# Performance work log

Measured on AMD Instinct MI355X. Metric: run time of the kernel, lower is better.

## Reference

```python
import jax, jax.numpy as jnp
import numpy as np

B, LQ, LK, D = 16, 2048, 2048, 64
TEMPERATURE = 8.0


def setup_inputs() -> dict:
    key = jax.random.key(0)
    kq, kk, kv, kt, km = jax.random.split(key, 5)
    q = jax.random.normal(kq, (B, LQ, D), dtype=jnp.float32)
    k = jax.random.normal(kk, (B, LK, D), dtype=jnp.float32)
    v = jax.random.normal(kv, (B, LK, D), dtype=jnp.float32)
    # time differences are positive
    time_diff = jax.random.uniform(kt, (B, LQ, LK), dtype=jnp.float32)
    mask = jax.random.randint(km, (B, LQ, LK), 0, 2).astype(bool)
    time_plus_weight = jnp.zeros((1,), dtype=jnp.float32)
    time_mul_weight = jnp.ones((1,), dtype=jnp.float32)
    return {"q": q, "k": k, "v": v, "time_diff": time_diff, "mask": mask,
            "time_plus_weight": time_plus_weight, "time_mul_weight": time_mul_weight}


def reference(q, k, v, time_diff, mask, time_plus_weight, time_mul_weight):
    # attn = QK^T / temperature  -> [B, LQ, LK]
    attn = jnp.einsum("bqd,bkd->bqk", q, k) / TEMPERATURE
    # time-decay bias (global mean/max over the whole time_diff tensor)
    td = time_diff / jnp.mean(time_diff)
    td = td + jax.nn.softplus(time_plus_weight) * jnp.max(td)
    time_diff_weight = 1.0 / jnp.log(jnp.exp(jnp.float32(1.0)) + td)
    attn = attn + time_mul_weight * time_diff_weight
    attn = jnp.where(mask, jnp.float32(-1e10), attn)
    attn = jax.nn.softmax(attn, axis=2)
    # dropout is identity in eval / p-effective-0 reference
    output = jnp.einsum("bqk,bkd->bqd", attn, v)
    return (output, attn)
```

## Files before the change

### kernel.cpp

```cpp
#include <hip/hip_runtime.h>
#include <hip/hip_bf16.h>

#define B_N 16
#define LQ_N 2048
#define LK_N 2048
#define D_N 64

typedef __attribute__((ext_vector_type(8))) __bf16 bf16x8;
typedef __attribute__((ext_vector_type(4))) float f32x4;
typedef __attribute__((ext_vector_type(2))) unsigned u32x2;
typedef __attribute__((ext_vector_type(4))) unsigned u32x4;

__device__ __forceinline__ unsigned cvt_pk_bf16(float lo, float hi) {
  unsigned r;
  asm("v_cvt_pk_bf16_f32 %0, %1, %2" : "=v"(r) : "v"(lo), "v"(hi));
  return r;
}

__device__ __forceinline__ void gl_lds16(const float* g, float* l) {
  __builtin_amdgcn_global_load_lds(
      (const __attribute__((address_space(1))) void*)g,
      (__attribute__((address_space(3))) void*)l, 16, 0, 0);
}

#define WAIT_VMC(N)  do { asm volatile("s_waitcnt vmcnt(" #N ")" ::: "memory"); __builtin_amdgcn_sched_barrier(0); } while (0)
#define WAIT_LGKM0() do { asm volatile("s_waitcnt lgkmcnt(0)" ::: "memory");    __builtin_amdgcn_sched_barrier(0); } while (0)
#define SBAR()       __builtin_amdgcn_sched_barrier(0)

__global__ __launch_bounds__(256) void red1_kernel(const float* __restrict__ td,
                                                   float* __restrict__ ws) {
  const int tid = threadIdx.x;
  const int gid = blockIdx.x * 256 + tid;
  float s = 0.f, mx = -1e30f;
  const float4* p = reinterpret_cast<const float4*>(td);
  for (int i = gid; i < 16777216; i += 524288) {
    float4 x = p[i];
    s += (x.x + x.y) + (x.z + x.w);
    mx = fmaxf(mx, fmaxf(fmaxf(x.x, x.y), fmaxf(x.z, x.w)));
  }
#pragma unroll
  for (int m = 1; m < 64; m <<= 1) {
    s += __shfl_xor(s, m, 64);
    mx = fmaxf(mx, __shfl_xor(mx, m, 64));
  }
  __shared__ float ss[4], sm[4];
  if ((tid & 63) == 0) { ss[tid >> 6] = s; sm[tid >> 6] = mx; }
  __syncthreads();
  if (tid == 0) {
    ws[blockIdx.x]        = (ss[0] + ss[1]) + (ss[2] + ss[3]);
    ws[2048 + blockIdx.x] = fmaxf(fmaxf(sm[0], sm[1]), fmaxf(sm[2], sm[3]));
  }
}

__global__ __launch_bounds__(256) void red2_kernel(const float* __restrict__ tpw,
                                                   const unsigned* __restrict__ mku,
                                                   float* __restrict__ ws) {
  const int tid = threadIdx.x;
  double s = 0.0; float mx = -1e30f;
  for (int i = tid; i < 2048; i += 256) { s += (double)ws[i]; mx = fmaxf(mx, ws[2048 + i]); }
#pragma unroll
  for (int m = 1; m < 64; m <<= 1) {
    s += __shfl_xor(s, m, 64);
    mx = fmaxf(mx, __shfl_xor(mx, m, 64));
  }
  unsigned big = 0;
  for (int i = tid; i < 1024; i += 256) big |= (mku[i] > 1u) ? 1u : 0u;
  const int anyw = __any(big != 0);
  __shared__ double sd[4]; __shared__ float sm[4]; __shared__ int sa[4];
  if ((tid & 63) == 0) { sd[tid >> 6] = s; sm[tid >> 6] = mx; sa[tid >> 6] = anyw; }
  __syncthreads();
  if (tid == 0) {
    double tot = (sd[0] + sd[1]) + (sd[2] + sd[3]);
    float m4 = fmaxf(fmaxf(sm[0], sm[1]), fmaxf(sm[2], sm[3]));
    double mean = tot / 67108864.0;
    float inv_mean = (float)(1.0 / mean);
    float sp = log1pf(__expf(tpw[0]));
    ws[4096] = inv_mean;
    ws[4097] = sp * m4 * inv_mean;
    ws[4098] = (sa[0] | sa[1] | sa[2] | sa[3]) ? 1.f : 0.f;
    ws[4099] = 2.718281828459045f + sp * m4 * inv_mean;
  }
}

__global__ __launch_bounds__(512)
void attn_kernel(
    const float* __restrict__ q, const float* __restrict__ kp, const float* __restrict__ vp,
    const float* __restrict__ td, const unsigned char* __restrict__ maskb,
    const float* __restrict__ tmwp, const float* __restrict__ ws,
    float* __restrict__ out, float* __restrict__ attn) {

  __shared__ float regA[8][2][1024];
  __shared__ unsigned short Qsb[16 * 72];
  __shared__ unsigned short Ps[8][16 * 24];
  __shared__ float rsum[8][16];

  const int tid  = threadIdx.x;
  const int w    = tid >> 6;
  const int lane = tid & 63;
  const int lrow = lane & 15;
  const int lgrp = lane >> 4;

  const int b     = blockIdx.x >> 7;
  const int qbase = (blockIdx.x & 127) << 4;

  const float inv_mean = ws[4096];
  const float ec       = ws[4099];
  const float tmw      = tmwp[0];
  const float sc       = tmw * 2.0813689810056077f;
  const int   msh      = (ws[4098] != 0.f) ? 0 : 2;

  if (tid < 256) {
    const float qscale = 0.18033688011112042f;
    const int row = tid >> 4, c4 = (tid & 15) << 2;
    f32x4 x = *reinterpret_cast<const f32x4*>(q + ((size_t)(b * LQ_N + qbase + row) << 6) + c4);
    *reinterpret_cast<u32x2*>(&Qsb[row * 72 + c4]) =
        u32x2{ cvt_pk_bf16(x[0] * qscale, x[1] * qscale),
               cvt_pk_bf16(x[2] * qscale, x[3] * qscale) };
  }
  __syncthreads();

  const unsigned qrow = (unsigned)(b * LQ_N + qbase + lrow);
  const unsigned tdo0 = (qrow << 11) + (unsigned)(w * 16 + lgrp * 4);
  const unsigned kvo0 = ((unsigned)b << 17) + ((unsigned)w << 10);
  const unsigned pA = (lgrp << 6) + ((lrow ^ lgrp)       << 2);
  const unsigned pB = (lgrp << 6) + ((lrow ^ (lgrp + 4)) << 2);

  auto dma16 = [&](const float* src_base, int c, int pb) {
    const unsigned base = kvo0 + (unsigned)c * 8192u;
    gl_lds16(src_base + (base         + pA), &regA[w][pb][0]);
    gl_lds16(src_base + (base +  256u + pB), &regA[w][pb][256]);
    gl_lds16(src_base + (base +  512u + pA), &regA[w][pb][512]);
    gl_lds16(src_base + (base +  768u + pB), &regA[w][pb][768]);
  };

  auto ldtd = [&](int c, f32x4* tdv, unsigned* mk4) {
    const unsigned to = tdo0 + (unsigned)c * 128u;
    *tdv = __builtin_nontemporal_load(reinterpret_cast<const f32x4*>(td + to));
    if (msh == 0) {
      *mk4 = *reinterpret_cast<const unsigned*>(maskb + to);
    } else {
      u32x4 m = __builtin_nontemporal_load(
          reinterpret_cast<const u32x4*>(maskb + ((size_t)to << 2)));
      *mk4 = (m[0] & 1u) | ((m[1] & 1u) << 8) | ((m[2] & 1u) << 16) | ((m[3] & 1u) << 24);
    }
  };

  dma16(kp, 0, 0); SBAR();
  dma16(kp, 1, 1); SBAR();
  f32x4    tdb[2];
  unsigned mkb[2];
  ldtd(0, &tdb[0], &mkb[0]); SBAR();

  float rs = 0.f;
  u32x2 E[16];

#pragma unroll
  for (int c = 0; c < 16; ++c) {
    if (c == 0)       { WAIT_VMC(6); }
    else if (c == 15) { WAIT_VMC(4); }
    else              { WAIT_VMC(8); }

    f32x4 acc = {0.f, 0.f, 0.f, 0.f};
#pragma unroll
    for (int h = 0; h < 2; ++h) {
      const int g0 = (h * 8 + lgrp * 2 + 0) ^ (lrow & 7);
      const int g1 = (h * 8 + lgrp * 2 + 1) ^ (lrow & 7);
      f32x4 ka = *(const f32x4*)&regA[w][c & 1][lrow * 64 + g0 * 4];
      f32x4 kc = *(const f32x4*)&regA[w][c & 1][lrow * 64 + g1 * 4];
      bf16x8 qv = *(const bf16x8*)&Qsb[lrow * 72 + h * 32 + lgrp * 8];
      u32x4 kd = { cvt_pk_bf16(ka[0], ka[1]), cvt_pk_bf16(ka[2], ka[3]),
                   cvt_pk_bf16(kc[0], kc[1]), cvt_pk_bf16(kc[2], kc[3]) };
      acc = __builtin_amdgcn_mfma_f32_16x16x32_bf16(__builtin_bit_cast(bf16x8, kd), qv,
                                                    acc, 0, 0, 0);
    }
    WAIT_LGKM0();
    if (c < 14) { dma16(kp, c + 2, c & 1); SBAR(); }
    if (c < 15) { ldtd(c + 1, &tdb[(c + 1) & 1], &mkb[(c + 1) & 1]); SBAR(); }

    if (c <= 13)      { WAIT_VMC(6); }
    else if (c == 14) { WAIT_VMC(2); }
    else              { WAIT_VMC(0); }

    const f32x4    tv  = tdb[c & 1];
    const unsigned mk4 = mkb[c & 1];
    float e4[4];
#pragma unroll
    for (int i = 0; i < 4; ++i) {
      const float z  = __builtin_fmaf(tv[i], inv_mean, ec);
      const float l2 = __builtin_amdgcn_logf(z);
      const float r  = __builtin_amdgcn_rcpf(l2);
      const float sv = __builtin_fmaf(sc, r, acc[i]);
      const float e  = ((mk4 >> (8 * i)) & 0xffu) ? 0.f : __builtin_amdgcn_exp2f(sv);
      e4[i] = e;
      rs += e;
    }
    E[c] = u32x2{ cvt_pk_bf16(e4[0], e4[1]), cvt_pk_bf16(e4[2], e4[3]) };
  }

  dma16(vp, 0, 0); SBAR();
  dma16(vp, 1, 1); SBAR();

  rs += __shfl_xor(rs, 16, 64);
  rs += __shfl_xor(rs, 32, 64);
  if (lgrp == 0) rsum[w][lrow] = rs;
  __syncthreads();
  float invl;
  {
    float s = 0.f;
#pragma unroll
    for (int w2 = 0; w2 < 8; ++w2) s += rsum[w2][lrow];
    invl = __fdividef(1.f, s);
  }

  f32x4 oacc[4];
#pragma unroll
  for (int n = 0; n < 4; ++n) oacc[n] = {0.f, 0.f, 0.f, 0.f};

  const u32x4 zz = {0u, 0u, 0u, 0u};
#pragma unroll
  for (int c = 0; c < 16; ++c) {
    if (c == 0)       { WAIT_VMC(4); }
    else if (c == 1)  { WAIT_VMC(5); }
    else if (c == 15) { WAIT_VMC(2); }
    else              { WAIT_VMC(6); }

    const unsigned ex = E[c][0], ey = E[c][1];
    f32x4 pv;
    pv[0] = __uint_as_float(ex << 16)         * invl;
    pv[1] = __uint_as_float(ex & 0xffff0000u) * invl;
    pv[2] = __uint_as_float(ey << 16)         * invl;
    pv[3] = __uint_as_float(ey & 0xffff0000u) * invl;

    const unsigned d01 = cvt_pk_bf16(pv[0], pv[1]);
    const unsigned d23 = cvt_pk_bf16(pv[2], pv[3]);
    *reinterpret_cast<u32x2*>(&Ps[w][lrow * 24 + lgrp * 4]) = u32x2{ d01, d23 };

    bf16x8 pa;
    if (lgrp < 2) pa = *(const bf16x8*)&Ps[w][lrow * 24 + lgrp * 8];
    else          pa = __builtin_bit_cast(bf16x8, zz);

#pragma unroll
    for (int n = 0; n < 4; ++n) {
      u32x4 vd;
      if (lgrp < 2) {
        float vv[8];
#pragma unroll
        for (int e = 0; e < 8; ++e) {
          const int r    = lgrp * 8 + e;
          const int dcol = n * 16 + lrow;
          const int slot = (dcol >> 2) ^ (r & 7);
          vv[e] = regA[w][c & 1][r * 64 + slot * 4 + (dcol & 3)];
        }
        vd = u32x4{ cvt_pk_bf16(vv[0], vv[1]), cvt_pk_bf16(vv[2], vv[3]),
                    cvt_pk_bf16(vv[4], vv[5]), cvt_pk_bf16(vv[6], vv[7]) };
      } else {
        vd = zz;
      }
      oacc[n] = __builtin_amdgcn_mfma_f32_16x16x32_bf16(pa, __builtin_bit_cast(bf16x8, vd),
                                                        oacc[n], 0, 0, 0);
    }

    WAIT_LGKM0();
    if (c < 14) { dma16(vp, c + 2, c & 1); SBAR(); }

    __builtin_nontemporal_store(pv, reinterpret_cast<f32x4*>(attn + tdo0 + (unsigned)c * 128u));
  }

#pragma unroll
  for (int n = 0; n < 4; ++n)
#pragma unroll
    for (int i = 0; i < 4; ++i)
      regA[w][0][(lgrp * 4 + i) * 64 + n * 16 + lrow] = oacc[n][i];
  __syncthreads();
  for (int i2 = tid; i2 < 1024; i2 += 512) {
    float s = 0.f;
#pragma unroll
    for (int w2 = 0; w2 < 8; ++w2) s += regA[w2][0][i2];
    out[((size_t)(b * LQ_N + qbase) << 6) + i2] = s;
  }
}

extern "C" void kernel_launch(void* const* d_in, const int* in_sizes, int n_in,
                              void* d_out, int out_size, void* d_ws, size_t ws_size,
                              hipStream_t stream) {
  const float* q   = (const float*)d_in[0];
  const float* k   = (const float*)d_in[1];
  const float* v   = (const float*)d_in[2];
  const float* td  = (const float*)d_in[3];
  const unsigned char* mask = (const unsigned char*)d_in[4];
  const float* tpw = (const float*)d_in[5];
  const float* tmw = (const float*)d_in[6];
  float* out  = (float*)d_out;
  float* attn = out + (size_t)B_N * LQ_N * D_N;
  float* wsf  = (float*)d_ws;

  red1_kernel<<<2048, 256, 0, stream>>>(td, wsf);
  red2_kernel<<<1, 256, 0, stream>>>(tpw, (const unsigned*)mask, wsf);
  attn_kernel<<<2048, 512, 0, stream>>>(q, k, v, td, mask, tmw, wsf, out, attn);
}
```

Measured before the change: 322.2 us.

## Split attention into row-sum pass and recompute-emit pass

The fused attention kernel becomes two kernels. The first computes QK^T plus the time bias and writes only the softmax row sums to the workspace. The second recomputes the scores, normalizes them, writes attn and does the PV product, so the E register buffer, the double-buffered K/V LDS region and the shared Q staging are no longer needed. This cuts register and LDS pressure, which could raise occupancy, but it reads time_diff, mask and K twice and runs QK^T twice, adding a lot of global traffic on an already memory-bound problem.

```diff
diff --git a/kernel.cpp b/kernel.cpp
--- a/kernel.cpp
+++ b/kernel.cpp
@@ -26,6 +26,7 @@
 #define WAIT_VMC(N)  do { asm volatile("s_waitcnt vmcnt(" #N ")" ::: "memory"); __builtin_amdgcn_sched_barrier(0); } while (0)
 #define WAIT_LGKM0() do { asm volatile("s_waitcnt lgkmcnt(0)" ::: "memory");    __builtin_amdgcn_sched_barrier(0); } while (0)
 #define SBAR()       __builtin_amdgcn_sched_barrier(0)
+
 
 __global__ __launch_bounds__(256) void red1_kernel(const float* __restrict__ td,
                                                    float* __restrict__ ws) {
@@ -76,22 +77,18 @@
     float inv_mean = (float)(1.0 / mean);
     float sp = log1pf(__expf(tpw[0]));
     ws[4096] = inv_mean;
-    ws[4097] = sp * m4 * inv_mean;
     ws[4098] = (sa[0] | sa[1] | sa[2] | sa[3]) ? 1.f : 0.f;
     ws[4099] = 2.718281828459045f + sp * m4 * inv_mean;
   }
 }
 
 __global__ __launch_bounds__(512)
-void attn_kernel(
-    const float* __restrict__ q, const float* __restrict__ kp, const float* __restrict__ vp,
+void sum_kernel(
+    const float* __restrict__ q, const float* __restrict__ kp,
     const float* __restrict__ td, const unsigned char* __restrict__ maskb,
-    const float* __restrict__ tmwp, const float* __restrict__ ws,
-    float* __restrict__ out, float* __restrict__ attn) {
-
-  __shared__ float regA[8][2][1024];
-  __shared__ unsigned short Qsb[16 * 72];
-  __shared__ unsigned short Ps[8][16 * 24];
+    const float* __restrict__ tmwp, float* __restrict__ ws) {
+
+  __shared__ float Kb[8][1024];
   __shared__ float rsum[8][16];
 
   const int tid  = threadIdx.x;
@@ -109,30 +106,19 @@
   const float sc       = tmw * 2.0813689810056077f;
   const int   msh      = (ws[4098] != 0.f) ? 0 : 2;
 
-  if (tid < 256) {
-    const float qscale = 0.18033688011112042f;
-    const int row = tid >> 4, c4 = (tid & 15) << 2;
-    f32x4 x = *reinterpret_cast<const f32x4*>(q + ((size_t)(b * LQ_N + qbase + row) << 6) + c4);
-    *reinterpret_cast<u32x2*>(&Qsb[row * 72 + c4]) =
-        u32x2{ cvt_pk_bf16(x[0] * qscale, x[1] * qscale),
-               cvt_pk_bf16(x[2] * qscale, x[3] * qscale) };
-  }
-  __syncthreads();
-
   const unsigned qrow = (unsigned)(b * LQ_N + qbase + lrow);
   const unsigned tdo0 = (qrow << 11) + (unsigned)(w * 16 + lgrp * 4);
   const unsigned kvo0 = ((unsigned)b << 17) + ((unsigned)w << 10);
   const unsigned pA = (lgrp << 6) + ((lrow ^ lgrp)       << 2);
   const unsigned pB = (lgrp << 6) + ((lrow ^ (lgrp + 4)) << 2);
 
-  auto dma16 = [&](const float* src_base, int c, int pb) {
+  auto kdma = [&](int c) {
     const unsigned base = kvo0 + (unsigned)c * 8192u;
-    gl_lds16(src_base + (base         + pA), &regA[w][pb][0]);
-    gl_lds16(src_base + (base +  256u + pB), &regA[w][pb][256]);
-    gl_lds16(src_base + (base +  512u + pA), &regA[w][pb][512]);
-    gl_lds16(src_base + (base +  768u + pB), &regA[w][pb][768]);
+    gl_lds16(kp + (base         + pA), &Kb[w][0]);
+    gl_lds16(kp + (base +  256u + pB), &Kb[w][256]);
+    gl_lds16(kp + (base +  512u + pA), &Kb[w][512]);
+    gl_lds16(kp + (base +  768u + pB), &Kb[w][768]);
   };
-
   auto ldtd = [&](int c, f32x4* tdv, unsigned* mk4) {
     const unsigned to = tdo0 + (unsigned)c * 128u;
     *tdv = __builtin_nontemporal_load(reinterpret_cast<const f32x4*>(td + to));
@@ -145,45 +131,55 @@
     }
   };
 
-  dma16(kp, 0, 0); SBAR();
-  dma16(kp, 1, 1); SBAR();
+  const float* qb = q + ((size_t)qrow << 6);
+  f32x4 q0a = *reinterpret_cast<const f32x4*>(qb + lgrp * 8);
+  f32x4 q0b = *reinterpret_cast<const f32x4*>(qb + lgrp * 8 + 4);
+  f32x4 q1a = *reinterpret_cast<const f32x4*>(qb + 32 + lgrp * 8);
+  f32x4 q1b = *reinterpret_cast<const f32x4*>(qb + 32 + lgrp * 8 + 4);
+  SBAR();
+  kdma(0); SBAR();
   f32x4    tdb[2];
   unsigned mkb[2];
   ldtd(0, &tdb[0], &mkb[0]); SBAR();
+  ldtd(1, &tdb[1], &mkb[1]); SBAR();
+
+  WAIT_VMC(8);
+  const float qscale = 0.18033688011112042f;
+  bf16x8 qa[2];
+  {
+    u32x4 k0 = { cvt_pk_bf16(q0a[0]*qscale, q0a[1]*qscale), cvt_pk_bf16(q0a[2]*qscale, q0a[3]*qscale),
+                 cvt_pk_bf16(q0b[0]*qscale, q0b[1]*qscale), cvt_pk_bf16(q0b[2]*qscale, q0b[3]*qscale) };
+    u32x4 k1 = { cvt_pk_bf16(q1a[0]*qscale, q1a[1]*qscale), cvt_pk_bf16(q1a[2]*qscale, q1a[3]*qscale),
+                 cvt_pk_bf16(q1b[0]*qscale, q1b[1]*qscale), cvt_pk_bf16(q1b[2]*qscale, q1b[3]*qscale) };
+    qa[0] = __builtin_bit_cast(bf16x8, k0);
+    qa[1] = __builtin_bit_cast(bf16x8, k1);
+  }
 
   float rs = 0.f;
-  u32x2 E[16];
-
 #pragma unroll
   for (int c = 0; c < 16; ++c) {
-    if (c == 0)       { WAIT_VMC(6); }
-    else if (c == 15) { WAIT_VMC(4); }
-    else              { WAIT_VMC(8); }
+    if (c == 0)       { WAIT_VMC(4); }
+    else if (c == 15) { WAIT_VMC(0); }
+    else              { WAIT_VMC(2); }
 
     f32x4 acc = {0.f, 0.f, 0.f, 0.f};
 #pragma unroll
     for (int h = 0; h < 2; ++h) {
       const int g0 = (h * 8 + lgrp * 2 + 0) ^ (lrow & 7);
       const int g1 = (h * 8 + lgrp * 2 + 1) ^ (lrow & 7);
-      f32x4 ka = *(const f32x4*)&regA[w][c & 1][lrow * 64 + g0 * 4];
-      f32x4 kc = *(const f32x4*)&regA[w][c & 1][lrow * 64 + g1 * 4];
-      bf16x8 qv = *(const bf16x8*)&Qsb[lrow * 72 + h * 32 + lgrp * 8];
+      f32x4 ka = *(const f32x4*)&Kb[w][lrow * 64 + g0 * 4];
+      f32x4 kc = *(const f32x4*)&Kb[w][lrow * 64 + g1 * 4];
       u32x4 kd = { cvt_pk_bf16(ka[0], ka[1]), cvt_pk_bf16(ka[2], ka[3]),
                    cvt_pk_bf16(kc[0], kc[1]), cvt_pk_bf16(kc[2], kc[3]) };
-      acc = __builtin_amdgcn_mfma_f32_16x16x32_bf16(__builtin_bit_cast(bf16x8, kd), qv,
+      acc = __builtin_amdgcn_mfma_f32_16x16x32_bf16(__builtin_bit_cast(bf16x8, kd), qa[h],
                                                     acc, 0, 0, 0);
     }
     WAIT_LGKM0();
-    if (c < 14) { dma16(kp, c + 2, c & 1); SBAR(); }
-    if (c < 15) { ldtd(c + 1, &tdb[(c + 1) & 1], &mkb[(c + 1) & 1]); SBAR(); }
-
-    if (c <= 13)      { WAIT_VMC(6); }
-    else if (c == 14) { WAIT_VMC(2); }
-    else              { WAIT_VMC(0); }
+    if (c < 15) { kdma(c + 1); SBAR(); }
+    if (c == 0) { WAIT_VMC(6); }
 
     const f32x4    tv  = tdb[c & 1];
     const unsigned mk4 = mkb[c & 1];
-    float e4[4];
 #pragma unroll
     for (int i = 0; i < 4; ++i) {
       const float z  = __builtin_fmaf(tv[i], inv_mean, ec);
@@ -191,53 +187,157 @@
       const float r  = __builtin_amdgcn_rcpf(l2);
       const float sv = __builtin_fmaf(sc, r, acc[i]);
       const float e  = ((mk4 >> (8 * i)) & 0xffu) ? 0.f : __builtin_amdgcn_exp2f(sv);
-      e4[i] = e;
       rs += e;
     }
-    E[c] = u32x2{ cvt_pk_bf16(e4[0], e4[1]), cvt_pk_bf16(e4[2], e4[3]) };
-  }
-
-  dma16(vp, 0, 0); SBAR();
-  dma16(vp, 1, 1); SBAR();
+    if (c < 14) { ldtd(c + 2, &tdb[c & 1], &mkb[c & 1]); SBAR(); }
+  }
 
   rs += __shfl_xor(rs, 16, 64);
   rs += __shfl_xor(rs, 32, 64);
   if (lgrp == 0) rsum[w][lrow] = rs;
   __syncthreads();
-  float invl;
+  if (tid < 16) {
+    float s = 0.f;
+#pragma unroll
+    for (int w2 = 0; w2 < 8; ++w2) s += rsum[w2][tid];
+    ws[8192 + (unsigned)(b * LQ_N + qbase) + tid] = s;
+  }
+}
+
+__global__ __launch_bounds__(512)
+void emit_kernel(
+    const float* __restrict__ q, const float* __restrict__ kp, const float* __restrict__ vp,
+    const float* __restrict__ td, const unsigned char* __restrict__ maskb,
+    const float* __restrict__ tmwp, const float* __restrict__ ws,
+    float* __restrict__ out, float* __restrict__ attn) {
+
+  __shared__ float Kb[8][1024];
+  __shared__ float Vb[8][1024];
+  __shared__ unsigned short Ps[8][16 * 24];
+
+  const int tid  = threadIdx.x;
+  const int w    = tid >> 6;
+  const int lane = tid & 63;
+  const int lrow = lane & 15;
+  const int lgrp = lane >> 4;
+
+  const int b     = blockIdx.x >> 7;
+  const int qbase = (blockIdx.x & 127) << 4;
+
+  const float inv_mean = ws[4096];
+  const float ec       = ws[4099];
+  const float tmw      = tmwp[0];
+  const float sc       = tmw * 2.0813689810056077f;
+  const int   msh      = (ws[4098] != 0.f) ? 0 : 2;
+
+  const unsigned qrow = (unsigned)(b * LQ_N + qbase + lrow);
+  const unsigned tdo0 = (qrow << 11) + (unsigned)(w * 16 + lgrp * 4);
+  const unsigned kvo0 = ((unsigned)b << 17) + ((unsigned)w << 10);
+  const unsigned pA = (lgrp << 6) + ((lrow ^ lgrp)       << 2);
+  const unsigned pB = (lgrp << 6) + ((lrow ^ (lgrp + 4)) << 2);
+
+  auto kdma = [&](int c) {
+    const unsigned base = kvo0 + (unsigned)c * 8192u;
+    gl_lds16(kp + (base         + pA), &Kb[w][0]);
+    gl_lds16(kp + (base +  256u + pB), &Kb[w][256]);
+    gl_lds16(kp + (base +  512u + pA), &Kb[w][512]);
+    gl_lds16(kp + (base +  768u + pB), &Kb[w][768]);
+  };
+  auto vdma = [&](int c) {
+    const unsigned base = kvo0 + (unsigned)c * 8192u;
+    gl_lds16(vp + (base         + pA), &Vb[w][0]);
+    gl_lds16(vp + (base +  256u + pB), &Vb[w][256]);
+    gl_lds16(vp + (base +  512u + pA), &Vb[w][512]);
+    gl_lds16(vp + (base +  768u + pB), &Vb[w][768]);
+  };
+  auto ldtd = [&](int c, f32x4* tdv, unsigned* mk4) {
+    const unsigned to = tdo0 + (unsigned)c * 128u;
+    *tdv = __builtin_nontemporal_load(reinterpret_cast<const f32x4*>(td + to));
+    if (msh == 0) {
+      *mk4 = *reinterpret_cast<const unsigned*>(maskb + to);
+    } else {
+      u32x4 m = __builtin_nontemporal_load(
+          reinterpret_cast<const u32x4*>(maskb + ((size_t)to << 2)));
+      *mk4 = (m[0] & 1u) | ((m[1] & 1u) << 8) | ((m[2] & 1u) << 16) | ((m[3] & 1u) << 24);
+    }
+  };
+
+  const float* qb = q + ((size_t)qrow << 6);
+  f32x4 q0a = *reinterpret_cast<const f32x4*>(qb + lgrp * 8);
+  f32x4 q0b = *reinterpret_cast<const f32x4*>(qb + lgrp * 8 + 4);
+  f32x4 q1a = *reinterpret_cast<const f32x4*>(qb + 32 + lgrp * 8);
+  f32x4 q1b = *reinterpret_cast<const f32x4*>(qb + 32 + lgrp * 8 + 4);
+  const float rsv = ws[8192 + qrow];
+  SBAR();
+  kdma(0); SBAR();
+  vdma(0); SBAR();
+  f32x4    tdb[2];
+  unsigned mkb[2];
+  ldtd(0, &tdb[0], &mkb[0]); SBAR();
+  ldtd(1, &tdb[1], &mkb[1]); SBAR();
+
+  WAIT_VMC(12);
+  const float invl = __fdividef(1.f, rsv);
+  const float qscale = 0.18033688011112042f;
+  bf16x8 qa[2];
   {
-    float s = 0.f;
-#pragma unroll
-    for (int w2 = 0; w2 < 8; ++w2) s += rsum[w2][lrow];
-    invl = __fdividef(1.f, s);
+    u32x4 k0 = { cvt_pk_bf16(q0a[0]*qscale, q0a[1]*qscale), cvt_pk_bf16(q0a[2]*qscale, q0a[3]*qscale),
+                 cvt_pk_bf16(q0b[0]*qscale, q0b[1]*qscale), cvt_pk_bf16(q0b[2]*qscale, q0b[3]*qscale) };
+    u32x4 k1 = { cvt_pk_bf16(q1a[0]*qscale, q1a[1]*qscale), cvt_pk_bf16(q1a[2]*qscale, q1a[3]*qscale),
+                 cvt_pk_bf16(q1b[0]*qscale, q1b[1]*qscale), cvt_pk_bf16(q1b[2]*qscale, q1b[3]*qscale) };
+    qa[0] = __builtin_bit_cast(bf16x8, k0);
+    qa[1] = __builtin_bit_cast(bf16x8, k1);
   }
 
   f32x4 oacc[4];
 #pragma unroll
   for (int n = 0; n < 4; ++n) oacc[n] = {0.f, 0.f, 0.f, 0.f};
-
   const u32x4 zz = {0u, 0u, 0u, 0u};
+
 #pragma unroll
   for (int c = 0; c < 16; ++c) {
-    if (c == 0)       { WAIT_VMC(4); }
-    else if (c == 1)  { WAIT_VMC(5); }
-    else if (c == 15) { WAIT_VMC(2); }
-    else              { WAIT_VMC(6); }
-
-    const unsigned ex = E[c][0], ey = E[c][1];
+    if (c == 0)       { WAIT_VMC(8); }
+    else if (c == 15) { WAIT_VMC(5); }
+    else              { WAIT_VMC(7); }
+
+    f32x4 acc = {0.f, 0.f, 0.f, 0.f};
+#pragma unroll
+    for (int h = 0; h < 2; ++h) {
+      const int g0 = (h * 8 + lgrp * 2 + 0) ^ (lrow & 7);
+      const int g1 = (h * 8 + lgrp * 2 + 1) ^ (lrow & 7);
+      f32x4 ka = *(const f32x4*)&Kb[w][lrow * 64 + g0 * 4];
+      f32x4 kc = *(const f32x4*)&Kb[w][lrow * 64 + g1 * 4];
+      u32x4 kd = { cvt_pk_bf16(ka[0], ka[1]), cvt_pk_bf16(ka[2], ka[3]),
+                   cvt_pk_bf16(kc[0], kc[1]), cvt_pk_bf16(kc[2], kc[3]) };
+      acc = __builtin_amdgcn_mfma_f32_16x16x32_bf16(__builtin_bit_cast(bf16x8, kd), qa[h],
+                                                    acc, 0, 0, 0);
+    }
+    WAIT_LGKM0();
+    if (c < 15) { kdma(c + 1); SBAR(); }
+    if (c == 0) { WAIT_VMC(6); }
+
+    const f32x4    tv  = tdb[c & 1];
+    const unsigned mk4 = mkb[c & 1];
     f32x4 pv;
-    pv[0] = __uint_as_float(ex << 16)         * invl;
-    pv[1] = __uint_as_float(ex & 0xffff0000u) * invl;
-    pv[2] = __uint_as_float(ey << 16)         * invl;
-    pv[3] = __uint_as_float(ey & 0xffff0000u) * invl;
+#pragma unroll
+    for (int i = 0; i < 4; ++i) {
+      const float z  = __builtin_fmaf(tv[i], inv_mean, ec);
+      const float l2 = __builtin_amdgcn_logf(z);
+      const float r  = __builtin_amdgcn_rcpf(l2);
+      const float sv = __builtin_fmaf(sc, r, acc[i]);
+      const float e  = ((mk4 >> (8 * i)) & 0xffu) ? 0.f : __builtin_amdgcn_exp2f(sv);
+      pv[i] = e * invl;
+    }
 
     const unsigned d01 = cvt_pk_bf16(pv[0], pv[1]);
     const unsigned d23 = cvt_pk_bf16(pv[2], pv[3]);
     *reinterpret_cast<u32x2*>(&Ps[w][lrow * 24 + lgrp * 4]) = u32x2{ d01, d23 };
-
     bf16x8 pa;
     if (lgrp < 2) pa = *(const bf16x8*)&Ps[w][lrow * 24 + lgrp * 8];
     else          pa = __builtin_bit_cast(bf16x8, zz);
+
+    if (c == 15)     { WAIT_VMC(1); }
+    else if (c >= 1) { WAIT_VMC(7); }
 
 #pragma unroll
     for (int n = 0; n < 4; ++n) {
@@ -249,7 +349,7 @@
           const int r    = lgrp * 8 + e;
           const int dcol = n * 16 + lrow;
           const int slot = (dcol >> 2) ^ (r & 7);
-          vv[e] = regA[w][c & 1][r * 64 + slot * 4 + (dcol & 3)];
+          vv[e] = Vb[w][r * 64 + slot * 4 + (dcol & 3)];
         }
         vd = u32x4{ cvt_pk_bf16(vv[0], vv[1]), cvt_pk_bf16(vv[2], vv[3]),
                     cvt_pk_bf16(vv[4], vv[5]), cvt_pk_bf16(vv[6], vv[7]) };
@@ -259,23 +359,24 @@
       oacc[n] = __builtin_amdgcn_mfma_f32_16x16x32_bf16(pa, __builtin_bit_cast(bf16x8, vd),
                                                         oacc[n], 0, 0, 0);
     }
-
     WAIT_LGKM0();
-    if (c < 14) { dma16(vp, c + 2, c & 1); SBAR(); }
+    if (c < 15) { vdma(c + 1); SBAR(); }
+    if (c < 14) { ldtd(c + 2, &tdb[c & 1], &mkb[c & 1]); SBAR(); }
 
     __builtin_nontemporal_store(pv, reinterpret_cast<f32x4*>(attn + tdo0 + (unsigned)c * 128u));
   }
 
+  __syncthreads();
 #pragma unroll
   for (int n = 0; n < 4; ++n)
 #pragma unroll
     for (int i = 0; i < 4; ++i)
-      regA[w][0][(lgrp * 4 + i) * 64 + n * 16 + lrow] = oacc[n][i];
+      Kb[w][(lgrp * 4 + i) * 64 + n * 16 + lrow] = oacc[n][i];
   __syncthreads();
   for (int i2 = tid; i2 < 1024; i2 += 512) {
     float s = 0.f;
 #pragma unroll
-    for (int w2 = 0; w2 < 8; ++w2) s += regA[w2][0][i2];
+    for (int w2 = 0; w2 < 8; ++w2) s += Kb[w2][i2];
     out[((size_t)(b * LQ_N + qbase) << 6) + i2] = s;
   }
 }
@@ -296,5 +397,6 @@
 
   red1_kernel<<<2048, 256, 0, stream>>>(td, wsf);
   red2_kernel<<<1, 256, 0, stream>>>(tpw, (const unsigned*)mask, wsf);
-  attn_kernel<<<2048, 512, 0, stream>>>(q, k, v, td, mask, tmw, wsf, out, attn);
-}
+  sum_kernel<<<2048, 512, 0, stream>>>(q, k, td, mask, tmw, wsf);
+  emit_kernel<<<2048, 512, 0, stream>>>(q, k, v, td, mask, tmw, wsf, out, attn);
+}
```

New measurement: 532.5 us. 1.65x slower.
